# Kernel tuning notes

Hardware: AMD Instinct MI355X
Metric: run time of the kernel (lower is better)

Reference implementation:

```python
import jax, jax.numpy as jnp
import numpy as np

HIDDEN = 2048
HEADS = 16
HEAD_DIM = HIDDEN // HEADS          # 128
HALF = HEAD_DIM // 2                # 64
LATENT = HIDDEN // 4                # 512 (compression_ratio=4)
ROPE_BASE = 10000.0


def _rope_cos_sin(seq_len):
    # LlamaRotaryEmbedding with dim=HALF
    inv_freq = 1.0 / (ROPE_BASE ** (jnp.arange(0, HALF, 2, dtype=jnp.float32) / HALF))
    t = jnp.arange(seq_len, dtype=jnp.float32)
    freqs = jnp.einsum('i,j->ij', t, inv_freq)          # [S, HALF/2]
    emb = jnp.concatenate([freqs, freqs], axis=-1)       # [S, HALF]
    cos = jnp.cos(emb)[None, :, None, :]                 # [1,S,1,HALF]
    sin = jnp.sin(emb)[None, :, None, :]
    return cos, sin


def _rotate_half(x):
    x1, x2 = jnp.split(x, 2, axis=-1)
    return jnp.concatenate([-x2, x1], axis=-1)


def _apply_rope(x, cos, sin):
    return x * cos + _rotate_half(x) * sin


def setup_inputs() -> dict:
    key = jax.random.key(0)
    ks = jax.random.split(key, 10)
    B, S = 2, 2048
    std = 0.02
    inp = {
        'x':        jax.random.normal(ks[0], (B, S, HIDDEN), jnp.float32),
        # weights stored as [in, out] (transposed torch Linear weight)
        'W_kv_d':   jax.random.normal(ks[1], (HIDDEN, LATENT), jnp.float32) * std,
        'W_q_d':    jax.random.normal(ks[2], (HIDDEN, LATENT), jnp.float32) * std,
        'W_k_u':    jax.random.normal(ks[3], (LATENT, HEADS * HALF), jnp.float32) * std,
        'W_q_u':    jax.random.normal(ks[4], (LATENT, HEADS * HALF), jnp.float32) * std,
        'W_v_u':    jax.random.normal(ks[5], (LATENT, HIDDEN), jnp.float32) * std,
        'W_rope_k': jax.random.normal(ks[6], (HIDDEN, HIDDEN // 2), jnp.float32) * std,
        'W_rope_q': jax.random.normal(ks[7], (LATENT, HIDDEN // 2), jnp.float32) * std,
        'W_o':      jax.random.normal(ks[8], (HIDDEN, HIDDEN), jnp.float32) * std,
    }
    return inp


def reference(x, W_kv_d, W_q_d, W_k_u, W_q_u, W_v_u, W_rope_k, W_rope_q, W_o):
    B, S, _ = x.shape
    kv_latent = x @ W_kv_d                      # [B,S,LATENT]
    q_latent = x @ W_q_d                        # [B,S,LATENT]

    k = (kv_latent @ W_k_u).reshape(B, S, HEADS, HALF)
    q = (q_latent @ W_q_u).reshape(B, S, HEADS, HALF)
    v = (kv_latent @ W_v_u).reshape(B, S, HEADS, HEAD_DIM)

    q_rope = (q_latent @ W_rope_q).reshape(B, S, HEADS, HALF)
    k_rope = (x @ W_rope_k).reshape(B, S, HEADS, HALF)

    cos, sin = _rope_cos_sin(S)
    k_rope = _apply_rope(k_rope, cos, sin)
    q_rope = _apply_rope(q_rope, cos, sin)

    q = jnp.concatenate([q, q_rope], axis=-1)   # [B,S,H,HEAD_DIM]
    k = jnp.concatenate([k, k_rope], axis=-1)

    scale = 1.0 / jnp.sqrt(jnp.float32(HEAD_DIM))
    scores = jnp.einsum('bqhd,bkhd->bhqk', q, k) * scale   # [B,H,S,S]
    causal = jnp.tril(jnp.ones((S, S), dtype=bool))
    scores = jnp.where(causal[None, None], scores, jnp.float32(-1e30))
    attn = jax.nn.softmax(scores, axis=-1)
    y = jnp.einsum('bhqk,bkhd->bqhd', attn, v).reshape(B, S, HIDDEN)
    return y @ W_o
```

## Files before the change

### kernel.cpp

```cpp
#include <hip/hip_runtime.h>
#include <hip/hip_bf16.h>

typedef __hip_bfloat16 bf16;
typedef __attribute__((ext_vector_type(8))) short short8;
typedef __attribute__((ext_vector_type(4))) float f32x4;

#define AS1 __attribute__((address_space(1)))
#define AS3 __attribute__((address_space(3)))

__device__ __forceinline__ void gload_lds16(const bf16* gp, bf16* lp) {
  __builtin_amdgcn_global_load_lds((const AS1 void*)gp, (AS3 void*)lp, 16, 0, 0);
}

__device__ __forceinline__ float fast_exp2(float x) {
#if __has_builtin(__builtin_amdgcn_exp2f)
  return __builtin_amdgcn_exp2f(x);
#else
  return exp2f(x);
#endif
}

__device__ __forceinline__ void store_c(bf16* C, size_t idx, float v) { C[idx] = __float2bfloat16(v); }
__device__ __forceinline__ void store_c(float* C, size_t idx, float v) { C[idx] = v; }

struct __align__(8) b16x4 { bf16 a, b, c, d; };

__global__ void cvt_f32_bf16(const float* __restrict__ in, bf16* __restrict__ out) {
  const int i = (blockIdx.x * 256 + threadIdx.x) * 4;
  const float4 v = *(const float4*)(in + i);
  out[i + 0] = __float2bfloat16(v.x);
  out[i + 1] = __float2bfloat16(v.y);
  out[i + 2] = __float2bfloat16(v.z);
  out[i + 3] = __float2bfloat16(v.w);
}

__global__ void rope_tab_kernel(float2* __restrict__ ctab) {
  const int idx = blockIdx.x * 256 + threadIdx.x;
  const int i = idx & 31;
  const int s = idx >> 5;
  const float inv = fast_exp2(-(float)i * 0.41524101186092029f);
  const float ang = (float)s * inv;
  ctab[idx] = make_float2(cosf(ang), sinf(ang));
}

struct PrepArgs {
  const float* src[8];
  bf16* dst[8];
  int R[8], C[8], cum[8];
};

__global__ void prep_kernel(PrepArgs a) {
  __shared__ bf16 t[32][33];
  const int blk = blockIdx.x;
  int e = 0;
  while (e < 7 && blk >= a.cum[e]) ++e;
  const int lt = blk - (e ? a.cum[e - 1] : 0);
  const int R = a.R[e], C = a.C[e];
  const int tpr = C >> 5;
  const int bx = lt % tpr, by = lt / tpr;
  const float* in = a.src[e];
  bf16* out = a.dst[e];
  const int c0 = bx * 32, r0 = by * 32;
  const int tx = threadIdx.x, ty = threadIdx.y;
  for (int i = 0; i < 4; ++i)
    t[ty + 8 * i][tx] = __float2bfloat16(in[(size_t)(r0 + ty + 8 * i) * C + c0 + tx]);
  __syncthreads();
  for (int i = 0; i < 4; ++i)
    out[(size_t)(c0 + ty + 8 * i) * R + r0 + tx] = t[tx][ty + 8 * i];
}

template <typename CT, int MODE>
__global__ void gemm_bt(const bf16* __restrict__ A, int lda,
                        const bf16* __restrict__ Bt,
                        CT* __restrict__ C, bf16* __restrict__ C2, int ldc,
                        int K, const float2* __restrict__ ctab)
{
  __shared__ __align__(16) bf16 As[128 * 32];
  __shared__ __align__(16) bf16 Bs[128 * 32];
  const int tid  = threadIdx.x;
  const int wave = tid >> 6, lane = tid & 63;
  const int quad = lane >> 4, l16 = lane & 15;
  const int m0 = blockIdx.y * 128, n0 = blockIdx.x * 128;
  const int wm = (wave >> 1) * 64, wn = (wave & 1) * 64;

  f32x4 acc[4][4];
#pragma unroll
  for (int i = 0; i < 4; ++i)
#pragma unroll
    for (int j = 0; j < 4; ++j) acc[i][j] = (f32x4){0.f, 0.f, 0.f, 0.f};

  const int r1  = tid >> 2;
  const int ks1 = (tid & 3) * 8;

  for (int k0 = 0; k0 < K; k0 += 32) {
    gload_lds16(A  + (size_t)(m0 + r1)      * lda + k0 + ks1, &As[tid * 8]);
    gload_lds16(A  + (size_t)(m0 + r1 + 64) * lda + k0 + ks1, &As[(tid + 256) * 8]);
    gload_lds16(Bt + (size_t)(n0 + r1)      * K   + k0 + ks1, &Bs[tid * 8]);
    gload_lds16(Bt + (size_t)(n0 + r1 + 64) * K   + k0 + ks1, &Bs[(tid + 256) * 8]);
    __syncthreads();

    short8 af[4], bf_[4];
#pragma unroll
    for (int mt = 0; mt < 4; ++mt)
      af[mt] = *(const short8*)&As[(wm + mt * 16 + l16) * 32 + quad * 8];
#pragma unroll
    for (int nt = 0; nt < 4; ++nt)
      bf_[nt] = *(const short8*)&Bs[(wn + nt * 16 + l16) * 32 + quad * 8];
#pragma unroll
    for (int mt = 0; mt < 4; ++mt)
#pragma unroll
      for (int nt = 0; nt < 4; ++nt)
        acc[mt][nt] = __builtin_amdgcn_mfma_f32_16x16x32_bf16(af[mt], bf_[nt], acc[mt][nt], 0, 0, 0);
    __syncthreads();
  }

  if (MODE == 0) {
#pragma unroll
    for (int mt = 0; mt < 4; ++mt) {
      const int row = m0 + wm + mt * 16 + quad * 4;
#pragma unroll
      for (int nt = 0; nt < 4; ++nt) {
        const int cn = n0 + wn + nt * 16 + l16;
        const f32x4 v = acc[mt][nt];
#pragma unroll
        for (int r = 0; r < 4; ++r)
          store_c(C, (size_t)(row + r) * ldc + cn, v[r]);
      }
    }
  } else if (MODE == 4) {
    if (n0 < 1024) {
#pragma unroll
      for (int mt = 0; mt < 4; ++mt) {
        const int row = m0 + wm + mt * 16 + quad * 4;
#pragma unroll
        for (int nt = 0; nt < 4; ++nt) {
          const int cn = n0 + wn + nt * 16 + l16;
          const f32x4 v = acc[mt][nt];
#pragma unroll
          for (int r = 0; r < 4; ++r)
            store_c(C, (size_t)(row + r) * 1024 + cn, v[r]);
        }
      }
    } else {
#pragma unroll
      for (int mt = 0; mt < 4; ++mt) {
        const int row = m0 + wm + mt * 16 + quad * 4;
        f32x4 w[4];
#pragma unroll
        for (int nt = 0; nt < 4; ++nt) w[nt] = acc[mt][nt];
#pragma unroll
        for (int r = 0; r < 4; ++r) {
          const int s = (row + r) & 2047;
          const float2 cs0 = ctab[(s << 5) + l16];
          const float2 cs1 = ctab[(s << 5) + 16 + l16];
          const float x1a = w[0][r], x2a = w[2][r];
          const float x1b = w[1][r], x2b = w[3][r];
          w[0][r] = x1a * cs0.x - x2a * cs0.y;
          w[2][r] = x2a * cs0.x + x1a * cs0.y;
          w[1][r] = x1b * cs1.x - x2b * cs1.y;
          w[3][r] = x2b * cs1.x + x1b * cs1.y;
        }
#pragma unroll
        for (int nt = 0; nt < 4; ++nt) {
          const int cn2 = n0 + wn + nt * 16 + l16 - 1024;
          const int g = ((cn2 >> 6) << 7) + 64 + (cn2 & 63);
#pragma unroll
          for (int r = 0; r < 4; ++r)
            C2[(size_t)(row + r) * 2048 + g] = __float2bfloat16(w[nt][r]);
        }
      }
    }
  }
}

__global__ void gemm_up_fused(const bf16* __restrict__ latcat,
                              const bf16* __restrict__ wtUP,
                              const bf16* __restrict__ wtQcat,
                              bf16* __restrict__ vT, bf16* __restrict__ kfull,
                              bf16* __restrict__ qfull,
                              const float2* __restrict__ ctab)
{
  const bool is2 = (blockIdx.x >= 24);
  const bf16* A  = latcat + (is2 ? 512 : 0);
  const bf16* Bt = is2 ? wtQcat : wtUP;
  const int n0 = (is2 ? (int)blockIdx.x - 24 : (int)blockIdx.x) * 128;
  const int K = 512, lda = 1024;

  __shared__ __align__(16) bf16 As[128 * 32];
  __shared__ __align__(16) bf16 Bs[128 * 32];
  const int tid  = threadIdx.x;
  const int wave = tid >> 6, lane = tid & 63;
  const int quad = lane >> 4, l16 = lane & 15;
  const int m0 = blockIdx.y * 128;
  const int wm = (wave >> 1) * 64, wn = (wave & 1) * 64;

  f32x4 acc[4][4];
#pragma unroll
  for (int i = 0; i < 4; ++i)
#pragma unroll
    for (int j = 0; j < 4; ++j) acc[i][j] = (f32x4){0.f, 0.f, 0.f, 0.f};

  const int r1  = tid >> 2;
  const int ks1 = (tid & 3) * 8;

  for (int k0 = 0; k0 < K; k0 += 32) {
    gload_lds16(A  + (size_t)(m0 + r1)      * lda + k0 + ks1, &As[tid * 8]);
    gload_lds16(A  + (size_t)(m0 + r1 + 64) * lda + k0 + ks1, &As[(tid + 256) * 8]);
    gload_lds16(Bt + (size_t)(n0 + r1)      * K   + k0 + ks1, &Bs[tid * 8]);
    gload_lds16(Bt + (size_t)(n0 + r1 + 64) * K   + k0 + ks1, &Bs[(tid + 256) * 8]);
    __syncthreads();

    short8 af[4], bf_[4];
#pragma unroll
    for (int mt = 0; mt < 4; ++mt)
      af[mt] = *(const short8*)&As[(wm + mt * 16 + l16) * 32 + quad * 8];
#pragma unroll
    for (int nt = 0; nt < 4; ++nt)
      bf_[nt] = *(const short8*)&Bs[(wn + nt * 16 + l16) * 32 + quad * 8];
#pragma unroll
    for (int mt = 0; mt < 4; ++mt)
#pragma unroll
      for (int nt = 0; nt < 4; ++nt)
        acc[mt][nt] = __builtin_amdgcn_mfma_f32_16x16x32_bf16(af[mt], bf_[nt], acc[mt][nt], 0, 0, 0);
    __syncthreads();
  }

  if (is2) {
    if (n0 < 1024) {
#pragma unroll
      for (int mt = 0; mt < 4; ++mt) {
        const int row = m0 + wm + mt * 16 + quad * 4;
#pragma unroll
        for (int nt = 0; nt < 4; ++nt) {
          const int cn = n0 + wn + nt * 16 + l16;
          const int g = (((cn >> 6) & 15) << 7) + ((cn >> 10) << 6) + (cn & 63);
          const f32x4 v = acc[mt][nt];
#pragma unroll
          for (int r = 0; r < 4; ++r)
            qfull[(size_t)(row + r) * 2048 + g] = __float2bfloat16(v[r]);
        }
      }
    } else {
#pragma unroll
      for (int mt = 0; mt < 4; ++mt) {
        const int row = m0 + wm + mt * 16 + quad * 4;
        f32x4 w[4];
#pragma unroll
        for (int nt = 0; nt < 4; ++nt) w[nt] = acc[mt][nt];
#pragma unroll
        for (int r = 0; r < 4; ++r) {
          const int s = (row + r) & 2047;
          const float2 cs0 = ctab[(s << 5) + l16];
          const float2 cs1 = ctab[(s << 5) + 16 + l16];
          const float x1a = w[0][r], x2a = w[2][r];
          const float x1b = w[1][r], x2b = w[3][r];
          w[0][r] = x1a * cs0.x - x2a * cs0.y;
          w[2][r] = x2a * cs0.x + x1a * cs0.y;
          w[1][r] = x1b * cs1.x - x2b * cs1.y;
          w[3][r] = x2b * cs1.x + x1b * cs1.y;
        }
#pragma unroll
        for (int nt = 0; nt < 4; ++nt) {
          const int cn = n0 + wn + nt * 16 + l16;
          const int g = (((cn >> 6) & 15) << 7) + ((cn >> 10) << 6) + (cn & 63);
#pragma unroll
          for (int r = 0; r < 4; ++r)
            qfull[(size_t)(row + r) * 2048 + g] = __float2bfloat16(w[nt][r]);
        }
      }
    }
  } else {
#pragma unroll
    for (int mt = 0; mt < 4; ++mt) {
      const int row = m0 + wm + mt * 16 + quad * 4;
#pragma unroll
      for (int nt = 0; nt < 4; ++nt) {
        const int cn = n0 + wn + nt * 16 + l16;
        const f32x4 v = acc[mt][nt];
        if (cn < 1024) {
          const int g = ((cn >> 6) << 7) + (cn & 63);
#pragma unroll
          for (int r = 0; r < 4; ++r)
            kfull[(size_t)(row + r) * 2048 + g] = __float2bfloat16(v[r]);
        } else {
          const int cn2 = cn - 1024;
          const int bb = row >> 11, s0 = row & 2047;
          b16x4 pk;
          pk.a = __float2bfloat16(v[0]); pk.b = __float2bfloat16(v[1]);
          pk.c = __float2bfloat16(v[2]); pk.d = __float2bfloat16(v[3]);
          *(b16x4*)(vT + ((size_t)(bb * 2048 + cn2)) * 2048 + s0) = pk;
        }
      }
    }
  }
}

__global__ __launch_bounds__(256, 2) void attn7_kernel(
    const bf16* __restrict__ Q, const bf16* __restrict__ Kf,
    const bf16* __restrict__ VT, bf16* __restrict__ Y)
{
  __shared__ __align__(16) bf16 Ks[64 * 128];
  __shared__ __align__(16) bf16 VTs[128 * 64];
  __shared__ __align__(16) bf16 Ps[4 * 32 * 64];
  const int tid  = threadIdx.x;
  const int wave = tid >> 6, lane = tid & 63;
  const int quad = lane >> 4, l16 = lane & 15;
  const int bh = blockIdx.x;
  const int yy = blockIdx.y;
  const int aa = yy & 7;
  const int qt = (yy >> 3) ? (15 - aa) : aa;
  const size_t kqbase = ((size_t)(bh >> 4) * 2048) * 2048 + (bh & 15) * 128;
  const size_t vtbase = (size_t)bh * 128 * 2048;
  const float C2 = 0.08838834764831845f * 1.4426950408889634f;
  const float MNEG = -30.0f;

  short8 ones;
#pragma unroll
  for (int i = 0; i < 8; ++i) ones[i] = (short)0x3F80;

  const int krow = tid >> 4, kcol = (tid & 15) * 8;
  const int vrow = tid >> 3, vcol = (tid & 7) * 8;

  const int q0 = qt * 128;
  const int T = 2 * qt + 2;
  const int wq0 = q0 + wave * 32;
  const int psbase = wave * (32 * 64);

  short8 qf[2][4];
#pragma unroll
  for (int m = 0; m < 2; ++m) {
    const bf16* qp = Q + kqbase + (size_t)(wq0 + m * 16 + l16) * 2048 + quad * 8;
#pragma unroll
    for (int kc = 0; kc < 4; ++kc) qf[m][kc] = *(const short8*)(qp + kc * 32);
  }
  f32x4 o[2][8];
#pragma unroll
  for (int m = 0; m < 2; ++m)
#pragma unroll
    for (int i = 0; i < 8; ++i) o[m][i] = (f32x4){0, 0, 0, 0};
  f32x4 lacc[2];
  lacc[0] = (f32x4){0, 0, 0, 0};
  lacc[1] = (f32x4){0, 0, 0, 0};

  short8 kg[4], vg[4];
#pragma unroll
  for (int i = 0; i < 4; ++i)
    kg[i] = *(const short8*)(Kf + kqbase + (size_t)(krow + i * 16) * 2048 + kcol);
#pragma unroll
  for (int i = 0; i < 4; ++i)
    vg[i] = *(const short8*)(VT + vtbase + (size_t)(vrow + i * 32) * 2048 + vcol);

  for (int t = 0; t < T; ++t) {
    const int k0 = t * 64;
    __syncthreads();
#pragma unroll
    for (int i = 0; i < 4; ++i) {
      const int rw = krow + i * 16;
      *(short8*)&Ks[rw * 128 + (kcol ^ ((rw & 7) * 8))] = kg[i];
    }
#pragma unroll
    for (int i = 0; i < 4; ++i) {
      const int rw = vrow + i * 32;
      *(short8*)&VTs[rw * 64 + (vcol ^ ((rw & 7) * 8))] = vg[i];
    }
    __syncthreads();
    if (t + 1 < T) {
      const int kn = k0 + 64;
#pragma unroll
      for (int i = 0; i < 4; ++i)
        kg[i] = *(const short8*)(Kf + kqbase + (size_t)(kn + krow + i * 16) * 2048 + kcol);
#pragma unroll
      for (int i = 0; i < 4; ++i)
        vg[i] = *(const short8*)(VT + vtbase + (size_t)(vrow + i * 32) * 2048 + kn + vcol);
    }

    if (k0 <= wq0 + 31) {
      f32x4 sf[2][4];
#pragma unroll
      for (int m = 0; m < 2; ++m)
#pragma unroll
        for (int kt = 0; kt < 4; ++kt) sf[m][kt] = (f32x4){0, 0, 0, 0};
#pragma unroll
      for (int kt = 0; kt < 4; ++kt) {
#pragma unroll
        for (int kc = 0; kc < 4; ++kc) {
          const short8 bfr = *(const short8*)&Ks[(kt * 16 + l16) * 128 +
                                                ((kc * 32 + quad * 8) ^ ((l16 & 7) * 8))];
          sf[0][kt] = __builtin_amdgcn_mfma_f32_16x16x32_bf16(qf[0][kc], bfr, sf[0][kt], 0, 0, 0);
          sf[1][kt] = __builtin_amdgcn_mfma_f32_16x16x32_bf16(qf[1][kc], bfr, sf[1][kt], 0, 0, 0);
        }
      }
#pragma unroll
      for (int m = 0; m < 2; ++m) {
        const int row0m = wq0 + m * 16 + quad * 4;
        if (k0 + 63 > row0m) {
#pragma unroll
          for (int kt = 0; kt < 4; ++kt) {
            const int col = k0 + kt * 16 + l16;
#pragma unroll
            for (int r = 0; r < 4; ++r)
              sf[m][kt][r] = (col > row0m + r) ? -3e38f : sf[m][kt][r];
          }
        }
      }
#pragma unroll
      for (int m = 0; m < 2; ++m)
#pragma unroll
        for (int kt = 0; kt < 4; ++kt)
#pragma unroll
          for (int r = 0; r < 4; ++r) {
            const float p = fast_exp2(__builtin_fmaf(sf[m][kt][r], C2, MNEG));
            const int prow = m * 16 + quad * 4 + r;
            const int pcol = (kt * 16 + l16) ^ (quad * 16);
            Ps[psbase + prow * 64 + pcol] = __float2bfloat16(p);
          }
      asm volatile("s_waitcnt lgkmcnt(0)" ::: "memory");
#pragma unroll
      for (int kc = 0; kc < 2; ++kc) {
        short8 ap[2];
#pragma unroll
        for (int m = 0; m < 2; ++m) {
          const int acol = (kc * 32 + quad * 8) ^ (((l16 >> 2) & 3) * 16);
          ap[m] = *(const short8*)&Ps[psbase + (m * 16 + l16) * 64 + acol];
          lacc[m] = __builtin_amdgcn_mfma_f32_16x16x32_bf16(ap[m], ones, lacc[m], 0, 0, 0);
        }
#pragma unroll
        for (int dt = 0; dt < 8; ++dt) {
          const short8 vb = *(const short8*)&VTs[(dt * 16 + l16) * 64 +
                                                ((kc * 32 + quad * 8) ^ ((l16 & 7) * 8))];
          o[0][dt] = __builtin_amdgcn_mfma_f32_16x16x32_bf16(ap[0], vb, o[0][dt], 0, 0, 0);
          o[1][dt] = __builtin_amdgcn_mfma_f32_16x16x32_bf16(ap[1], vb, o[1][dt], 0, 0, 0);
        }
      }
    }
  }

#pragma unroll
  for (int m = 0; m < 2; ++m) {
    const int row0m = wq0 + m * 16 + quad * 4;
#pragma unroll
    for (int r = 0; r < 4; ++r) {
      const float inv = 1.0f / lacc[m][r];
#pragma unroll
      for (int dt = 0; dt < 8; ++dt)
        Y[kqbase + (size_t)(row0m + r) * 2048 + dt * 16 + l16] =
            __float2bfloat16(o[m][dt][r] * inv);
    }
  }
}

extern "C" void kernel_launch(void* const* d_in, const int* in_sizes, int n_in,
                              void* d_out, int out_size, void* d_ws, size_t ws_size,
                              hipStream_t stream)
{
  const float* x      = (const float*)d_in[0];
  const float* Wkvd   = (const float*)d_in[1];
  const float* Wqd    = (const float*)d_in[2];
  const float* Wku    = (const float*)d_in[3];
  const float* Wqu    = (const float*)d_in[4];
  const float* Wvu    = (const float*)d_in[5];
  const float* Wropek = (const float*)d_in[6];
  const float* Wropeq = (const float*)d_in[7];
  const float* Wo     = (const float*)d_in[8];

  char* ws = (char*)d_ws;
  size_t off = 0;
  auto alloc = [&](size_t elems) {
    bf16* p = (bf16*)(ws + off);
    off += ((elems * sizeof(bf16) + 255) & ~(size_t)255);
    return p;
  };
  bf16* wtX    = alloc((size_t)2048 * 2048);
  bf16* wtUP   = alloc((size_t)3072 * 512);
  bf16* wtQcat = alloc((size_t)2048 * 512);
  bf16* latcat = alloc((size_t)4096 * 1024);
  bf16* wt_o   = alloc((size_t)2048 * 2048);
  bf16* xbf    = alloc((size_t)4096 * 2048);
  bf16* qfull  = alloc((size_t)4096 * 2048);
  bf16* kfull  = alloc((size_t)4096 * 2048);
  float2* ctab = (float2*)alloc((size_t)65536 * 4);
  bf16* ybuf   = (bf16*)ws;
  bf16* vT     = (bf16*)d_out;
  (void)ws_size; (void)in_sizes; (void)n_in; (void)out_size;

  rope_tab_kernel<<<256, 256, 0, stream>>>(ctab);
  cvt_f32_bf16<<<8192, 256, 0, stream>>>(x, xbf);

  PrepArgs pa;
  const float* srcs[8] = {Wkvd, Wqd, Wropek, Wku, Wvu, Wqu, Wropeq, Wo};
  bf16* dsts[8] = {wtX, wtX + (size_t)512 * 2048, wtX + (size_t)1024 * 2048,
                   wtUP, wtUP + (size_t)1024 * 512,
                   wtQcat, wtQcat + (size_t)1024 * 512, wt_o};
  const int Rs[8] = {2048, 2048, 2048, 512, 512, 512, 512, 2048};
  const int Cs[8] = {512, 512, 1024, 1024, 2048, 1024, 1024, 2048};
  int cum = 0;
  for (int e = 0; e < 8; ++e) {
    pa.src[e] = srcs[e]; pa.dst[e] = dsts[e]; pa.R[e] = Rs[e]; pa.C[e] = Cs[e];
    cum += (Rs[e] >> 5) * (Cs[e] >> 5);
    pa.cum[e] = cum;
  }
  prep_kernel<<<cum, dim3(32, 8), 0, stream>>>(pa);

  gemm_bt<bf16, 4><<<dim3(16, 32), 256, 0, stream>>>(xbf, 2048, wtX, latcat, kfull, 1024, 2048, ctab);
  gemm_up_fused<<<dim3(40, 32), 256, 0, stream>>>(latcat, wtUP, wtQcat, vT, kfull, qfull, ctab);

  attn7_kernel<<<dim3(32, 16), 256, 0, stream>>>(qfull, kfull, vT, ybuf);
  gemm_bt<float, 0><<<dim3(16, 32), 256, 0, stream>>>(ybuf, 2048, wt_o, (float*)d_out, (bf16*)nullptr, 2048, 2048, ctab);
}
```

Baseline: 326.9 us.

## Double-buffer LDS tiles in projection GEMMs to overlap loads with MFMA

```diff
diff --git a/kernel.cpp b/kernel.cpp
--- a/kernel.cpp
+++ b/kernel.cpp
@@ -75,8 +75,8 @@
                         CT* __restrict__ C, bf16* __restrict__ C2, int ldc,
                         int K, const float2* __restrict__ ctab)
 {
-  __shared__ __align__(16) bf16 As[128 * 32];
-  __shared__ __align__(16) bf16 Bs[128 * 32];
+  __shared__ __align__(16) bf16 As[2][128 * 32];
+  __shared__ __align__(16) bf16 Bs[2][128 * 32];
   const int tid  = threadIdx.x;
   const int wave = tid >> 6, lane = tid & 63;
   const int quad = lane >> 4, l16 = lane & 15;
@@ -92,26 +92,40 @@
   const int r1  = tid >> 2;
   const int ks1 = (tid & 3) * 8;
 
+  gload_lds16(A  + (size_t)(m0 + r1)      * lda + ks1, &As[0][tid * 8]);
+  gload_lds16(A  + (size_t)(m0 + r1 + 64) * lda + ks1, &As[0][(tid + 256) * 8]);
+  gload_lds16(Bt + (size_t)(n0 + r1)      * K   + ks1, &Bs[0][tid * 8]);
+  gload_lds16(Bt + (size_t)(n0 + r1 + 64) * K   + ks1, &Bs[0][(tid + 256) * 8]);
+
+  int cur = 0;
   for (int k0 = 0; k0 < K; k0 += 32) {
-    gload_lds16(A  + (size_t)(m0 + r1)      * lda + k0 + ks1, &As[tid * 8]);
-    gload_lds16(A  + (size_t)(m0 + r1 + 64) * lda + k0 + ks1, &As[(tid + 256) * 8]);
-    gload_lds16(Bt + (size_t)(n0 + r1)      * K   + k0 + ks1, &Bs[tid * 8]);
-    gload_lds16(Bt + (size_t)(n0 + r1 + 64) * K   + k0 + ks1, &Bs[(tid + 256) * 8]);
-    __syncthreads();
+    if (k0 + 32 < K) {
+      const int kn = k0 + 32;
+      const int nxt = cur ^ 1;
+      gload_lds16(A  + (size_t)(m0 + r1)      * lda + kn + ks1, &As[nxt][tid * 8]);
+      gload_lds16(A  + (size_t)(m0 + r1 + 64) * lda + kn + ks1, &As[nxt][(tid + 256) * 8]);
+      gload_lds16(Bt + (size_t)(n0 + r1)      * K   + kn + ks1, &Bs[nxt][tid * 8]);
+      gload_lds16(Bt + (size_t)(n0 + r1 + 64) * K   + kn + ks1, &Bs[nxt][(tid + 256) * 8]);
+      asm volatile("s_waitcnt vmcnt(4)" ::: "memory");
+    } else {
+      asm volatile("s_waitcnt vmcnt(0)" ::: "memory");
+    }
+    __builtin_amdgcn_s_barrier();
 
     short8 af[4], bf_[4];
 #pragma unroll
     for (int mt = 0; mt < 4; ++mt)
-      af[mt] = *(const short8*)&As[(wm + mt * 16 + l16) * 32 + quad * 8];
+      af[mt] = *(const short8*)&As[cur][(wm + mt * 16 + l16) * 32 + quad * 8];
 #pragma unroll
     for (int nt = 0; nt < 4; ++nt)
-      bf_[nt] = *(const short8*)&Bs[(wn + nt * 16 + l16) * 32 + quad * 8];
+      bf_[nt] = *(const short8*)&Bs[cur][(wn + nt * 16 + l16) * 32 + quad * 8];
 #pragma unroll
     for (int mt = 0; mt < 4; ++mt)
 #pragma unroll
       for (int nt = 0; nt < 4; ++nt)
         acc[mt][nt] = __builtin_amdgcn_mfma_f32_16x16x32_bf16(af[mt], bf_[nt], acc[mt][nt], 0, 0, 0);
-    __syncthreads();
+    __builtin_amdgcn_s_barrier();
+    cur ^= 1;
   }
 
   if (MODE == 0) {
@@ -186,8 +200,8 @@
   const int n0 = (is2 ? (int)blockIdx.x - 24 : (int)blockIdx.x) * 128;
   const int K = 512, lda = 1024;
 
-  __shared__ __align__(16) bf16 As[128 * 32];
-  __shared__ __align__(16) bf16 Bs[128 * 32];
+  __shared__ __align__(16) bf16 As[2][128 * 32];
+  __shared__ __align__(16) bf16 Bs[2][128 * 32];
   const int tid  = threadIdx.x;
   const int wave = tid >> 6, lane = tid & 63;
   const int quad = lane >> 4, l16 = lane & 15;
@@ -203,26 +217,40 @@
   const int r1  = tid >> 2;
   const int ks1 = (tid & 3) * 8;
 
+  gload_lds16(A  + (size_t)(m0 + r1)      * lda + ks1, &As[0][tid * 8]);
+  gload_lds16(A  + (size_t)(m0 + r1 + 64) * lda + ks1, &As[0][(tid + 256) * 8]);
+  gload_lds16(Bt + (size_t)(n0 + r1)      * K   + ks1, &Bs[0][tid * 8]);
+  gload_lds16(Bt + (size_t)(n0 + r1 + 64) * K   + ks1, &Bs[0][(tid + 256) * 8]);
+
+  int cur = 0;
   for (int k0 = 0; k0 < K; k0 += 32) {
-    gload_lds16(A  + (size_t)(m0 + r1)      * lda + k0 + ks1, &As[tid * 8]);
-    gload_lds16(A  + (size_t)(m0 + r1 + 64) * lda + k0 + ks1, &As[(tid + 256) * 8]);
-    gload_lds16(Bt + (size_t)(n0 + r1)      * K   + k0 + ks1, &Bs[tid * 8]);
-    gload_lds16(Bt + (size_t)(n0 + r1 + 64) * K   + k0 + ks1, &Bs[(tid + 256) * 8]);
-    __syncthreads();
+    if (k0 + 32 < K) {
+      const int kn = k0 + 32;
+      const int nxt = cur ^ 1;
+      gload_lds16(A  + (size_t)(m0 + r1)      * lda + kn + ks1, &As[nxt][tid * 8]);
+      gload_lds16(A  + (size_t)(m0 + r1 + 64) * lda + kn + ks1, &As[nxt][(tid + 256) * 8]);
+      gload_lds16(Bt + (size_t)(n0 + r1)      * K   + kn + ks1, &Bs[nxt][tid * 8]);
+      gload_lds16(Bt + (size_t)(n0 + r1 + 64) * K   + kn + ks1, &Bs[nxt][(tid + 256) * 8]);
+      asm volatile("s_waitcnt vmcnt(4)" ::: "memory");
+    } else {
+      asm volatile("s_waitcnt vmcnt(0)" ::: "memory");
+    }
+    __builtin_amdgcn_s_barrier();
 
     short8 af[4], bf_[4];
 #pragma unroll
     for (int mt = 0; mt < 4; ++mt)
-      af[mt] = *(const short8*)&As[(wm + mt * 16 + l16) * 32 + quad * 8];
+      af[mt] = *(const short8*)&As[cur][(wm + mt * 16 + l16) * 32 + quad * 8];
 #pragma unroll
     for (int nt = 0; nt < 4; ++nt)
-      bf_[nt] = *(const short8*)&Bs[(wn + nt * 16 + l16) * 32 + quad * 8];
+      bf_[nt] = *(const short8*)&Bs[cur][(wn + nt * 16 + l16) * 32 + quad * 8];
 #pragma unroll
     for (int mt = 0; mt < 4; ++mt)
 #pragma unroll
       for (int nt = 0; nt < 4; ++nt)
         acc[mt][nt] = __builtin_amdgcn_mfma_f32_16x16x32_bf16(af[mt], bf_[nt], acc[mt][nt], 0, 0, 0);
-    __syncthreads();
+    __builtin_amdgcn_s_barrier();
+    cur ^= 1;
   }
 
   if (is2) {
```

New measurement: 324.1 us. Within noise of the previous version (-0.9%).
